# Kernel optimization log

Hardware: AMD Instinct MI355X
Metric: run time of the kernel (lower is better)

## Reference

```python
import jax, jax.numpy as jnp
import numpy as np
import math


def _alibi_slopes(h):
    # h must be a power of 2 here (h=16); matches pow2slopes in the source
    start = 2.0 ** (-2.0 ** (-(math.log2(h) - 3.0)))
    return jnp.asarray([start ** (i + 1) for i in range(h)], dtype=jnp.float32)


def setup_inputs() -> dict:
    key = jax.random.key(0)
    ks = jax.random.split(key, 7)
    B, N, d, h, r = 2, 2048, 1024, 16, 32
    dk = d // h
    x = jax.random.normal(ks[0], (B, N, d), dtype=jnp.float32)
    # causal additive mask (standard usage of the optional `mask` arg)
    i = jnp.arange(N)[:, None]
    j = jnp.arange(N)[None, :]
    mask = jnp.where(j > i, jnp.float32(-1e9), jnp.float32(0.0))[None, None]  # [1,1,N,N]
    s = 1.0 / math.sqrt(d)
    Wq = jax.random.normal(ks[1], (d, d), dtype=jnp.float32) * s
    Wk = jax.random.normal(ks[2], (d, d), dtype=jnp.float32) * s
    Wv = jax.random.normal(ks[3], (d, d), dtype=jnp.float32) * s
    # orthogonal init of U, as in nn.init.orthogonal_
    U, _ = jnp.linalg.qr(jax.random.normal(ks[4], (dk, r), dtype=jnp.float32))
    Wproj = jax.random.normal(ks[5], (d, h * r), dtype=jnp.float32) * (1.0 / math.sqrt(h * r))
    return {"x": x, "mask": mask, "Wq": Wq, "Wk": Wk, "Wv": Wv, "U": U,
            "Wproj": Wproj, "rel_bias_tokens": N}


def reference(x, mask, Wq, Wk, Wv, U, Wproj, rel_bias_tokens):
    B, N, d = x.shape
    dk, r = U.shape
    h = d // dk

    def lowrank_proj(W):
        # Linear(d,d,bias=False) then per-head low-rank projection by U
        y = (x @ W.T).reshape(B, N, h, dk)          # [B,N,h,dk]
        return jnp.einsum('bnhk,kr->bhnr', y, U)     # [B,h,N,r]

    q = lowrank_proj(Wq)
    k = lowrank_proj(Wk)
    v = lowrank_proj(Wv)

    # scores scaled by sqrt(dk) (NOT sqrt(r)) -- faithful to source
    att = jnp.einsum('bhnr,bhmr->bhnm', q, k) / math.sqrt(dk)  # [B,h,N,N]

    # q_len == k_len branch: alibi bias + mask
    i = jnp.arange(rel_bias_tokens)[:, None]
    j = jnp.arange(rel_bias_tokens)[None, :]
    dist = jnp.maximum(j - i, 0).astype(att.dtype)             # clamp_min(0)
    slopes = _alibi_slopes(h)
    att = att + (-slopes[:, None, None] * dist)[None] + mask

    z = jnp.einsum('bhnm,bhmr->bhnr', jax.nn.softmax(att, axis=-1), v)
    z = z.transpose(0, 2, 1, 3).reshape(B, N, h * r)
    # dropout is identity in eval
    return z @ Wproj.T
```

## Files before the change

### kernel.cpp

```cpp
#include <hip/hip_runtime.h>
#include <hip/hip_bf16.h>
#include <stdint.h>

typedef unsigned short u16;
typedef __attribute__((ext_vector_type(4))) short short4v;
typedef __attribute__((ext_vector_type(8))) short short8;
typedef __attribute__((ext_vector_type(4))) float f32x4;

#define NB 2
#define NN 2048
#define ND 1024
#define NH 16
#define NR 32
#define NM (NB*NN)
#define NHR 512
#define NQKV 1536

static __device__ __forceinline__ u16 f2bf(float f) {
  union { float f; uint32_t u; } v; v.f = f;
  uint32_t r = v.u + 0x7fffu + ((v.u >> 16) & 1u);
  return (u16)(r >> 16);
}
static __device__ __forceinline__ u16 fastbf(float f) {
  union { float f; uint32_t u; } v; v.f = f;
  return (u16)((v.u + 0x8000u) >> 16);
}

typedef __attribute__((address_space(1))) unsigned int as1_u32;
typedef __attribute__((address_space(3))) unsigned int as3_u32;

static __device__ __forceinline__ void async_copy16(void* lds, const void* g) {
  __builtin_amdgcn_global_load_lds((as1_u32*)(uintptr_t)g,
                                   (as3_u32*)(uint32_t)(uintptr_t)lds,
                                   16, 0, 0);
}

__global__ void cast_f32_bf16(const float* __restrict__ in, u16* __restrict__ o,
                              int n8) {
  int i = blockIdx.x * 256 + threadIdx.x;
  if (i >= n8) return;
  const float4* p = (const float4*)in + (size_t)i * 2;
  float4 a = p[0], b = p[1];
  short8 v;
  v[0] = f2bf(a.x); v[1] = f2bf(a.y); v[2] = f2bf(a.z); v[3] = f2bf(a.w);
  v[4] = f2bf(b.x); v[5] = f2bf(b.y); v[6] = f2bf(b.z); v[7] = f2bf(b.w);
  *((short8*)o + i) = v;
}

__global__ __launch_bounds__(256, 2)
void build_wct(const float* __restrict__ Wq, const float* __restrict__ Wk,
               const float* __restrict__ Wv, const float* __restrict__ U,
               u16* __restrict__ WcT) {
  __shared__ float sU[64 * 32];
  const int tid = threadIdx.x;
  #pragma unroll
  for (int t = 0; t < 2; ++t)
    ((float4*)sU)[t * 256 + tid] = ((const float4*)U)[t * 256 + tid];
  __syncthreads();
  const int wh = blockIdx.y;
  const int w = wh >> 4, head = wh & 15;
  const float* W = (w == 0) ? Wq : (w == 1 ? Wk : Wv);
  const int i = blockIdx.x * 256 + tid;
  const float* Wcol = W + (size_t)head * 64 * ND + i;
  float acc[32];
  #pragma unroll
  for (int rr = 0; rr < 32; ++rr) acc[rr] = 0.f;
  for (int kk = 0; kk < 64; ++kk) {
    const float wv = Wcol[(size_t)kk * ND];
    const float4* u4 = (const float4*)&sU[kk * 32];
    #pragma unroll
    for (int r4 = 0; r4 < 8; ++r4) {
      float4 u = u4[r4];
      acc[r4 * 4 + 0] += wv * u.x;
      acc[r4 * 4 + 1] += wv * u.y;
      acc[r4 * 4 + 2] += wv * u.z;
      acc[r4 * 4 + 3] += wv * u.w;
    }
  }
  const float sc = (w == 0) ? 0.125f : 1.0f;
  const int colBase = w * 512 + head * 32;
  #pragma unroll
  for (int rr = 0; rr < 32; ++rr)
    WcT[(size_t)(colBase + rr) * ND + i] = f2bf(acc[rr] * sc);
}

template<int EPI>
__global__ __launch_bounds__(256, 2)
void gemm_bt(const u16* __restrict__ A, int lda,
             const u16* __restrict__ BT, int ldb, int K,
             u16* __restrict__ o0, u16* __restrict__ o1, u16* __restrict__ o2,
             float* __restrict__ fo) {
  __shared__ __align__(16) u16 lA[128 * 64];
  __shared__ __align__(16) u16 lB[128 * 64];
  const int tid = threadIdx.x;
  const int lane = tid & 63, quad = lane >> 4, l16 = lane & 15;
  const int wave = tid >> 6;
  const int wm = (wave >> 1) * 64, wn = (wave & 1) * 64;
  const int rowBase = blockIdx.y * 128, colBase = blockIdx.x * 128;

  f32x4 acc[4][4];
  #pragma unroll
  for (int i = 0; i < 4; ++i)
    #pragma unroll
    for (int j = 0; j < 4; ++j)
      acc[i][j] = (f32x4){0.f, 0.f, 0.f, 0.f};

  for (int kt = 0; kt < K; kt += 64) {
    #pragma unroll
    for (int it = 0; it < 4; ++it) {
      const int cid = it * 256 + tid;
      const int row = cid >> 3, pc = cid & 7;
      const int gc = pc ^ (row & 7);
      async_copy16(&lA[cid * 8], &A[(size_t)(rowBase + row) * lda + kt + gc * 8]);
      async_copy16(&lB[cid * 8], &BT[(size_t)(colBase + row) * ldb + kt + gc * 8]);
    }
    __syncthreads();
    #pragma unroll
    for (int ks = 0; ks < 64; ks += 32) {
      short8 fa[4], fb[4];
      #pragma unroll
      for (int t = 0; t < 4; ++t) {
        const int ra = wm + t * 16 + l16;
        const int pa = ((ks >> 3) + quad) ^ (ra & 7);
        fa[t] = *(const short8*)&lA[ra * 64 + pa * 8];
        const int rb = wn + t * 16 + l16;
        const int pb = ((ks >> 3) + quad) ^ (rb & 7);
        fb[t] = *(const short8*)&lB[rb * 64 + pb * 8];
      }
      #pragma unroll
      for (int mt = 0; mt < 4; ++mt)
        #pragma unroll
        for (int nt = 0; nt < 4; ++nt)
          acc[mt][nt] = __builtin_amdgcn_mfma_f32_16x16x32_bf16(
              fa[mt], fb[nt], acc[mt][nt], 0, 0, 0);
    }
    __syncthreads();
  }

  #pragma unroll
  for (int mt = 0; mt < 4; ++mt) {
    const int gr0 = rowBase + wm + mt * 16 + quad * 4;
    #pragma unroll
    for (int nt = 0; nt < 4; ++nt) {
      const int c = colBase + wn + nt * 16 + l16;
      #pragma unroll
      for (int j = 0; j < 4; ++j) {
        const float v = acc[mt][nt][j];
        const int row = gr0 + j;
        if (EPI == 0) {
          fo[(size_t)row * 1024 + c] = v;
        } else {
          const int b = row >> 11, n = row & (NN - 1);
          const int w = c >> 9, ch = c & 511, head = ch >> 5, rr = ch & 31;
          if (w == 0)
            o0[(size_t)(((b * NH + head) * NN + n)) * NR + rr] = f2bf(v);
          else if (w == 1)
            o1[(size_t)(((b * NH + head) * NN + n)) * NR + rr] = f2bf(v);
          else
            o2[(size_t)((b * NH + head) * NR + rr) * NN + n] = f2bf(v);
        }
      }
    }
  }
}

__global__ __launch_bounds__(256, 4)
void flash_attn(const u16* __restrict__ q, const u16* __restrict__ k,
                const u16* __restrict__ vt, u16* __restrict__ z) {
  __shared__ __align__(16) u16 lK[2][64 * 32];
  __shared__ __align__(16) u16 lV[2][32 * 64];
  const int bh = blockIdx.y;
  const int b = bh >> 4, head = bh & 15;
  const int tid = threadIdx.x;
  const int lane = tid & 63, quad = lane >> 4, l16 = lane & 15;
  const int wave = tid >> 6;
  const int qblk = gridDim.x - 1 - blockIdx.x;
  const int qb0 = qblk * 64;
  const int qbase = qb0 + wave * 16;
  const int qq = qbase + l16;

  const u16* qp = q  + (size_t)bh * NN * NR;
  const u16* kp = k  + (size_t)bh * NN * NR;
  const u16* vp = vt + (size_t)bh * NR * NN;

  const short8 bq = *(const short8*)&qp[(size_t)(qbase + l16) * NR + quad * 8];

  f32x4 Ot0 = (f32x4){0.f,0.f,0.f,0.f};
  f32x4 Ot1 = (f32x4){0.f,0.f,0.f,0.f};
  float ls = 0.f;

  const int krow = tid >> 2, kc = tid & 3;
  const int vrow = tid >> 3, vpc = tid & 7;
  const int vgc = vpc ^ (vrow & 7);

  #define STAGE(kt_, buf_) do {                                            \
    const int m0_ = (kt_) * 64;                                            \
    async_copy16(&lK[buf_][tid * 8], &kp[(size_t)(m0_ + krow) * NR + kc * 8]); \
    async_copy16(&lV[buf_][tid * 8], &vp[(size_t)vrow * NN + m0_ + vgc * 8]);  \
  } while (0)

  STAGE(0, 0);
  int buf = 0;
  for (int kt = 0; kt <= qblk; ++kt) {
    asm volatile("s_waitcnt vmcnt(0) lgkmcnt(0)" ::: "memory");
    __syncthreads();
    if (kt < qblk) STAGE(kt + 1, buf ^ 1);

    const int m0 = kt * 64;
    f32x4 s[4];
    const f32x4 zero = (f32x4){0.f,0.f,0.f,0.f};
    #pragma unroll
    for (int g = 0; g < 4; ++g) {
      const short8 ak = *(const short8*)&lK[buf][(16 * g + l16) * 32 + quad * 8];
      s[g] = __builtin_amdgcn_mfma_f32_16x16x32_bf16(ak, bq, zero, 0, 0, 0);
    }
    if (kt == qblk) {
      #pragma unroll
      for (int g = 0; g < 4; ++g)
        #pragma unroll
        for (int j = 0; j < 4; ++j)
          if (m0 + 16 * g + quad * 4 + j > qq) s[g][j] = -1e30f;
    }
    #pragma unroll
    for (int g = 0; g < 4; ++g) {
      const float p0 = __expf(s[g][0]), p1 = __expf(s[g][1]);
      const float p2 = __expf(s[g][2]), p3 = __expf(s[g][3]);
      ls += (p0 + p1) + (p2 + p3);
      short4v bp;
      bp[0] = fastbf(p0); bp[1] = fastbf(p1); bp[2] = fastbf(p2); bp[3] = fastbf(p3);
      const int c0 = 2 * g + (quad >> 1), off = (quad & 1) * 4;
      const short4v av0 = *(const short4v*)
          &lV[buf][l16 * 64 + ((c0 ^ (l16 & 7)) * 8) + off];
      const short4v av1 = *(const short4v*)
          &lV[buf][(16 + l16) * 64 + ((c0 ^ ((16 + l16) & 7)) * 8) + off];
      Ot0 = __builtin_amdgcn_mfma_f32_16x16x16bf16_1k(av0, bp, Ot0, 0, 0, 0);
      Ot1 = __builtin_amdgcn_mfma_f32_16x16x16bf16_1k(av1, bp, Ot1, 0, 0, 0);
    }
    asm volatile("s_waitcnt lgkmcnt(0)" ::: "memory");
    __syncthreads();
    buf ^= 1;
  }
  #undef STAGE

  ls += __shfl_xor(ls, 16);
  ls += __shfl_xor(ls, 32);
  const float inv = 1.f / ls;

  short4v o0, o1;
  #pragma unroll
  for (int j = 0; j < 4; ++j) {
    o0[j] = f2bf(Ot0[j] * inv);
    o1[j] = f2bf(Ot1[j] * inv);
  }
  u16* zr = z + (size_t)(b * NN + qq) * NHR + head * NR;
  *(short4v*)&zr[quad * 4]      = o0;
  *(short4v*)&zr[16 + quad * 4] = o1;
}

extern "C" void kernel_launch(void* const* d_in, const int* in_sizes, int n_in,
                              void* d_out, int out_size, void* d_ws, size_t ws_size,
                              hipStream_t stream) {
  const float* x     = (const float*)d_in[0];
  const float* Wq    = (const float*)d_in[2];
  const float* Wk    = (const float*)d_in[3];
  const float* Wv    = (const float*)d_in[4];
  const float* U     = (const float*)d_in[5];
  const float* Wproj = (const float*)d_in[6];
  float* out = (float*)d_out;

  u16* ws  = (u16*)d_ws;
  u16* xb  = ws;
  u16* z   = ws;
  u16* Wpb = ws + (size_t)4 * 1024 * 1024;
  u16* WcT = Wpb + (size_t)512 * 1024;
  u16* q   = ws + (size_t)6 * 1024 * 1024;
  u16* kk  = q  + (size_t)NB * NH * NN * NR;
  u16* vt  = kk + (size_t)NB * NH * NN * NR;

  cast_f32_bf16<<<(NM * ND / 8 + 255) / 256, 256, 0, stream>>>(x, xb, NM * ND / 8);
  cast_f32_bf16<<<(ND * NHR / 8 + 255) / 256, 256, 0, stream>>>(Wproj, Wpb, ND * NHR / 8);
  build_wct<<<dim3(ND / 256, 48), 256, 0, stream>>>(Wq, Wk, Wv, U, WcT);
  gemm_bt<1><<<dim3(NQKV / 128, NM / 128), 256, 0, stream>>>(
      xb, ND, WcT, ND, ND, q, kk, vt, nullptr);
  flash_attn<<<dim3(NN / 64, NB * NH), 256, 0, stream>>>(q, kk, vt, z);
  gemm_bt<0><<<dim3(ND / 128, NM / 128), 256, 0, stream>>>(
      z, NHR, Wpb, NHR, NHR, nullptr, nullptr, nullptr, out);
}
```

Measured before the change: 183.6 us.

## Process two query tiles per attention block and fuse prep kernels

Flash attention now handles 128 queries per block as two 64-row groups that share each staged K/V tile, halving K/V traffic and LDS staging per query. The three preprocessing launches (x cast, Wproj cast, combined weight build) are merged into one kernel dispatched by block index, cutting launch overhead. The trade-off is fewer attention blocks with more uneven causal work and higher register use.

```diff
diff --git a/kernel.cpp b/kernel.cpp
--- a/kernel.cpp
+++ b/kernel.cpp
@@ -35,53 +35,56 @@
                                    16, 0, 0);
 }
 
-__global__ void cast_f32_bf16(const float* __restrict__ in, u16* __restrict__ o,
-                              int n8) {
-  int i = blockIdx.x * 256 + threadIdx.x;
-  if (i >= n8) return;
-  const float4* p = (const float4*)in + (size_t)i * 2;
-  float4 a = p[0], b = p[1];
-  short8 v;
-  v[0] = f2bf(a.x); v[1] = f2bf(a.y); v[2] = f2bf(a.z); v[3] = f2bf(a.w);
-  v[4] = f2bf(b.x); v[5] = f2bf(b.y); v[6] = f2bf(b.z); v[7] = f2bf(b.w);
-  *((short8*)o + i) = v;
-}
-
 __global__ __launch_bounds__(256, 2)
-void build_wct(const float* __restrict__ Wq, const float* __restrict__ Wk,
-               const float* __restrict__ Wv, const float* __restrict__ U,
-               u16* __restrict__ WcT) {
+void prep(const float* __restrict__ x, const float* __restrict__ Wproj,
+          const float* __restrict__ Wq, const float* __restrict__ Wk,
+          const float* __restrict__ Wv, const float* __restrict__ U,
+          u16* __restrict__ xb, u16* __restrict__ Wpb, u16* __restrict__ WcT) {
   __shared__ float sU[64 * 32];
+  const int blk = blockIdx.x;
   const int tid = threadIdx.x;
-  #pragma unroll
-  for (int t = 0; t < 2; ++t)
-    ((float4*)sU)[t * 256 + tid] = ((const float4*)U)[t * 256 + tid];
-  __syncthreads();
-  const int wh = blockIdx.y;
-  const int w = wh >> 4, head = wh & 15;
-  const float* W = (w == 0) ? Wq : (w == 1 ? Wk : Wv);
-  const int i = blockIdx.x * 256 + tid;
-  const float* Wcol = W + (size_t)head * 64 * ND + i;
-  float acc[32];
-  #pragma unroll
-  for (int rr = 0; rr < 32; ++rr) acc[rr] = 0.f;
-  for (int kk = 0; kk < 64; ++kk) {
-    const float wv = Wcol[(size_t)kk * ND];
-    const float4* u4 = (const float4*)&sU[kk * 32];
-    #pragma unroll
-    for (int r4 = 0; r4 < 8; ++r4) {
-      float4 u = u4[r4];
-      acc[r4 * 4 + 0] += wv * u.x;
-      acc[r4 * 4 + 1] += wv * u.y;
-      acc[r4 * 4 + 2] += wv * u.z;
-      acc[r4 * 4 + 3] += wv * u.w;
-    }
-  }
-  const float sc = (w == 0) ? 0.125f : 1.0f;
-  const int colBase = w * 512 + head * 32;
-  #pragma unroll
-  for (int rr = 0; rr < 32; ++rr)
-    WcT[(size_t)(colBase + rr) * ND + i] = f2bf(acc[rr] * sc);
+  if (blk < 2304) {
+    const float* in = (blk < 2048) ? x : Wproj;
+    u16* o = (blk < 2048) ? xb : Wpb;
+    const int i = ((blk < 2048) ? blk : (blk - 2048)) * 256 + tid;
+    const float4* p = (const float4*)in + (size_t)i * 2;
+    float4 a = p[0], b2 = p[1];
+    short8 v;
+    v[0] = f2bf(a.x);  v[1] = f2bf(a.y);  v[2] = f2bf(a.z);  v[3] = f2bf(a.w);
+    v[4] = f2bf(b2.x); v[5] = f2bf(b2.y); v[6] = f2bf(b2.z); v[7] = f2bf(b2.w);
+    *((short8*)o + i) = v;
+  } else {
+    #pragma unroll
+    for (int t = 0; t < 2; ++t)
+      ((float4*)sU)[t * 256 + tid] = ((const float4*)U)[t * 256 + tid];
+    __syncthreads();
+    const int local = blk - 2304;
+    const int wh = local >> 2;
+    const int w = wh >> 4, head = wh & 15;
+    const float* W = (w == 0) ? Wq : (w == 1 ? Wk : Wv);
+    const int i = (local & 3) * 256 + tid;
+    const float* Wcol = W + (size_t)head * 64 * ND + i;
+    float acc[32];
+    #pragma unroll
+    for (int rr = 0; rr < 32; ++rr) acc[rr] = 0.f;
+    for (int kk = 0; kk < 64; ++kk) {
+      const float wv = Wcol[(size_t)kk * ND];
+      const float4* u4 = (const float4*)&sU[kk * 32];
+      #pragma unroll
+      for (int r4 = 0; r4 < 8; ++r4) {
+        float4 u = u4[r4];
+        acc[r4 * 4 + 0] += wv * u.x;
+        acc[r4 * 4 + 1] += wv * u.y;
+        acc[r4 * 4 + 2] += wv * u.z;
+        acc[r4 * 4 + 3] += wv * u.w;
+      }
+    }
+    const float sc = (w == 0) ? 0.125f : 1.0f;
+    const int colBase = w * 512 + head * 32;
+    #pragma unroll
+    for (int rr = 0; rr < 32; ++rr)
+      WcT[(size_t)(colBase + rr) * ND + i] = f2bf(acc[rr] * sc);
+  }
 }
 
 template<int EPI>
@@ -175,19 +178,20 @@
   const int lane = tid & 63, quad = lane >> 4, l16 = lane & 15;
   const int wave = tid >> 6;
   const int qblk = gridDim.x - 1 - blockIdx.x;
-  const int qb0 = qblk * 64;
-  const int qbase = qb0 + wave * 16;
-  const int qq = qbase + l16;
+  const int qb0 = qblk * 128;
+  const int qq1 = qb0 + 16 * wave + l16;
+  const int qq2 = qq1 + 64;
 
   const u16* qp = q  + (size_t)bh * NN * NR;
   const u16* kp = k  + (size_t)bh * NN * NR;
   const u16* vp = vt + (size_t)bh * NR * NN;
 
-  const short8 bq = *(const short8*)&qp[(size_t)(qbase + l16) * NR + quad * 8];
-
-  f32x4 Ot0 = (f32x4){0.f,0.f,0.f,0.f};
-  f32x4 Ot1 = (f32x4){0.f,0.f,0.f,0.f};
-  float ls = 0.f;
+  const short8 bq1 = *(const short8*)&qp[(size_t)qq1 * NR + quad * 8];
+  const short8 bq2 = *(const short8*)&qp[(size_t)qq2 * NR + quad * 8];
+
+  f32x4 O1a = (f32x4){0.f,0.f,0.f,0.f}, O1b = (f32x4){0.f,0.f,0.f,0.f};
+  f32x4 O2a = (f32x4){0.f,0.f,0.f,0.f}, O2b = (f32x4){0.f,0.f,0.f,0.f};
+  float ls1 = 0.f, ls2 = 0.f;
 
   const int krow = tid >> 2, kc = tid & 3;
   const int vrow = tid >> 3, vpc = tid & 7;
@@ -201,40 +205,66 @@
 
   STAGE(0, 0);
   int buf = 0;
-  for (int kt = 0; kt <= qblk; ++kt) {
+  const int ktmax = 2 * qblk + 1;
+  for (int kt = 0; kt <= ktmax; ++kt) {
     asm volatile("s_waitcnt vmcnt(0) lgkmcnt(0)" ::: "memory");
     __syncthreads();
-    if (kt < qblk) STAGE(kt + 1, buf ^ 1);
+    if (kt < ktmax) STAGE(kt + 1, buf ^ 1);
 
     const int m0 = kt * 64;
-    f32x4 s[4];
+    const bool g1on = (kt <= 2 * qblk);
     const f32x4 zero = (f32x4){0.f,0.f,0.f,0.f};
+    short8 ak[4];
+    #pragma unroll
+    for (int g = 0; g < 4; ++g)
+      ak[g] = *(const short8*)&lK[buf][(16 * g + l16) * 32 + quad * 8];
+
+    f32x4 s1[4], s2[4];
     #pragma unroll
     for (int g = 0; g < 4; ++g) {
-      const short8 ak = *(const short8*)&lK[buf][(16 * g + l16) * 32 + quad * 8];
-      s[g] = __builtin_amdgcn_mfma_f32_16x16x32_bf16(ak, bq, zero, 0, 0, 0);
-    }
-    if (kt == qblk) {
+      s2[g] = __builtin_amdgcn_mfma_f32_16x16x32_bf16(ak[g], bq2, zero, 0, 0, 0);
+      if (g1on)
+        s1[g] = __builtin_amdgcn_mfma_f32_16x16x32_bf16(ak[g], bq1, zero, 0, 0, 0);
+    }
+    if (kt == ktmax) {
       #pragma unroll
       for (int g = 0; g < 4; ++g)
         #pragma unroll
         for (int j = 0; j < 4; ++j)
-          if (m0 + 16 * g + quad * 4 + j > qq) s[g][j] = -1e30f;
+          if (m0 + 16 * g + quad * 4 + j > qq2) s2[g][j] = -1e30f;
+    }
+    if (kt == 2 * qblk) {
+      #pragma unroll
+      for (int g = 0; g < 4; ++g)
+        #pragma unroll
+        for (int j = 0; j < 4; ++j)
+          if (m0 + 16 * g + quad * 4 + j > qq1) s1[g][j] = -1e30f;
     }
     #pragma unroll
     for (int g = 0; g < 4; ++g) {
-      const float p0 = __expf(s[g][0]), p1 = __expf(s[g][1]);
-      const float p2 = __expf(s[g][2]), p3 = __expf(s[g][3]);
-      ls += (p0 + p1) + (p2 + p3);
-      short4v bp;
-      bp[0] = fastbf(p0); bp[1] = fastbf(p1); bp[2] = fastbf(p2); bp[3] = fastbf(p3);
       const int c0 = 2 * g + (quad >> 1), off = (quad & 1) * 4;
       const short4v av0 = *(const short4v*)
           &lV[buf][l16 * 64 + ((c0 ^ (l16 & 7)) * 8) + off];
       const short4v av1 = *(const short4v*)
           &lV[buf][(16 + l16) * 64 + ((c0 ^ ((16 + l16) & 7)) * 8) + off];
-      Ot0 = __builtin_amdgcn_mfma_f32_16x16x16bf16_1k(av0, bp, Ot0, 0, 0, 0);
-      Ot1 = __builtin_amdgcn_mfma_f32_16x16x16bf16_1k(av1, bp, Ot1, 0, 0, 0);
+      {
+        const float p0 = __expf(s2[g][0]), p1 = __expf(s2[g][1]);
+        const float p2 = __expf(s2[g][2]), p3 = __expf(s2[g][3]);
+        ls2 += (p0 + p1) + (p2 + p3);
+        short4v bp;
+        bp[0] = fastbf(p0); bp[1] = fastbf(p1); bp[2] = fastbf(p2); bp[3] = fastbf(p3);
+        O2a = __builtin_amdgcn_mfma_f32_16x16x16bf16_1k(av0, bp, O2a, 0, 0, 0);
+        O2b = __builtin_amdgcn_mfma_f32_16x16x16bf16_1k(av1, bp, O2b, 0, 0, 0);
+      }
+      if (g1on) {
+        const float p0 = __expf(s1[g][0]), p1 = __expf(s1[g][1]);
+        const float p2 = __expf(s1[g][2]), p3 = __expf(s1[g][3]);
+        ls1 += (p0 + p1) + (p2 + p3);
+        short4v bp;
+        bp[0] = fastbf(p0); bp[1] = fastbf(p1); bp[2] = fastbf(p2); bp[3] = fastbf(p3);
+        O1a = __builtin_amdgcn_mfma_f32_16x16x16bf16_1k(av0, bp, O1a, 0, 0, 0);
+        O1b = __builtin_amdgcn_mfma_f32_16x16x16bf16_1k(av1, bp, O1b, 0, 0, 0);
+      }
     }
     asm volatile("s_waitcnt lgkmcnt(0)" ::: "memory");
     __syncthreads();
@@ -242,19 +272,22 @@
   }
   #undef STAGE
 
-  ls += __shfl_xor(ls, 16);
-  ls += __shfl_xor(ls, 32);
-  const float inv = 1.f / ls;
-
-  short4v o0, o1;
+  ls1 += __shfl_xor(ls1, 16);  ls1 += __shfl_xor(ls1, 32);
+  ls2 += __shfl_xor(ls2, 16);  ls2 += __shfl_xor(ls2, 32);
+  const float inv1 = 1.f / ls1, inv2 = 1.f / ls2;
+
+  short4v o1a, o1b, o2a, o2b;
   #pragma unroll
   for (int j = 0; j < 4; ++j) {
-    o0[j] = f2bf(Ot0[j] * inv);
-    o1[j] = f2bf(Ot1[j] * inv);
-  }
-  u16* zr = z + (size_t)(b * NN + qq) * NHR + head * NR;
-  *(short4v*)&zr[quad * 4]      = o0;
-  *(short4v*)&zr[16 + quad * 4] = o1;
+    o1a[j] = f2bf(O1a[j] * inv1);  o1b[j] = f2bf(O1b[j] * inv1);
+    o2a[j] = f2bf(O2a[j] * inv2);  o2b[j] = f2bf(O2b[j] * inv2);
+  }
+  u16* zr1 = z + (size_t)(b * NN + qq1) * NHR + head * NR;
+  *(short4v*)&zr1[quad * 4]      = o1a;
+  *(short4v*)&zr1[16 + quad * 4] = o1b;
+  u16* zr2 = z + (size_t)(b * NN + qq2) * NHR + head * NR;
+  *(short4v*)&zr2[quad * 4]      = o2a;
+  *(short4v*)&zr2[16 + quad * 4] = o2b;
 }
 
 extern "C" void kernel_launch(void* const* d_in, const int* in_sizes, int n_in,
@@ -277,12 +310,10 @@
   u16* kk  = q  + (size_t)NB * NH * NN * NR;
   u16* vt  = kk + (size_t)NB * NH * NN * NR;
 
-  cast_f32_bf16<<<(NM * ND / 8 + 255) / 256, 256, 0, stream>>>(x, xb, NM * ND / 8);
-  cast_f32_bf16<<<(ND * NHR / 8 + 255) / 256, 256, 0, stream>>>(Wproj, Wpb, ND * NHR / 8);
-  build_wct<<<dim3(ND / 256, 48), 256, 0, stream>>>(Wq, Wk, Wv, U, WcT);
+  prep<<<2496, 256, 0, stream>>>(x, Wproj, Wq, Wk, Wv, U, xb, Wpb, WcT);
   gemm_bt<1><<<dim3(NQKV / 128, NM / 128), 256, 0, stream>>>(
       xb, ND, WcT, ND, ND, q, kk, vt, nullptr);
-  flash_attn<<<dim3(NN / 64, NB * NH), 256, 0, stream>>>(q, kk, vt, z);
+  flash_attn<<<dim3(NN / 128, NB * NH), 256, 0, stream>>>(q, kk, vt, z);
   gemm_bt<0><<<dim3(ND / 128, NM / 128), 256, 0, stream>>>(
       z, NHR, Wpb, NHR, NHR, nullptr, nullptr, nullptr, out);
 }
```

After: 185.5 us. Within noise of the previous version (+1.0%).
